# Kernel optimization log

Measured on AMD Instinct MI355X. Metric: run time of the kernel, lower is better.

## Reference

```python
import jax, jax.numpy as jnp
import numpy as np

B, NKV, NQ, D, H = 4, 2048, 1024, 1024, 16
HD = D // H


def setup_inputs() -> dict:
    key = jax.random.key(0)
    ks = jax.random.split(key, 9)
    s = 0.02
    return {
        "x": jax.random.normal(ks[0], (B, NKV, D), jnp.float32),
        "y": jax.random.normal(ks[1], (B, NQ, D), jnp.float32),
        "mask": jax.random.randint(ks[2], (B, NQ, NKV), 0, 2, jnp.int32),
        "W_kv": jax.random.normal(ks[3], (D, 2 * D), jnp.float32) * s,
        "b_kv": jnp.zeros((2 * D,), jnp.float32),
        "W_q": jax.random.normal(ks[4], (D, D), jnp.float32) * s,
        "b_q": jnp.zeros((D,), jnp.float32),
        "W_o": jax.random.normal(ks[5], (D, D), jnp.float32) * s,
        "b_o": jnp.zeros((D,), jnp.float32),
    }


def reference(x, y, mask, W_kv, b_kv, W_q, b_q, W_o, b_o):
    b, nkv, _ = x.shape
    nq = y.shape[1]
    kv = x @ W_kv + b_kv                                  # [B, NKV, 2D]
    q = y @ W_q + b_q                                     # [B, NQ, D]
    kv = kv.reshape(b, nkv, H, 2 * HD).transpose(0, 2, 1, 3)  # [B,H,NKV,2HD]
    q = q.reshape(b, nq, H, HD).transpose(0, 2, 1, 3)         # [B,H,NQ,HD]
    k, v = kv[..., :HD], kv[..., HD:]
    scores = jnp.einsum('bhqd,bhkd->bhqk', q, k) / jnp.sqrt(jnp.float32(HD))
    scores = jnp.where(mask[:, None, :, :] == 0, jnp.float32(-1e20), scores)
    attn = jax.nn.softmax(scores, axis=-1)
    vals = jnp.einsum('bhqk,bhkd->bhqd', attn, v)          # [B,H,NQ,HD]
    vals = vals.transpose(0, 2, 1, 3).reshape(b, nq, D)
    return vals @ W_o + b_o
```

## Files before the change

kernel.cpp:

```cpp
#include <hip/hip_runtime.h>
#include <hip/hip_bf16.h>
#include <math.h>

#define B_   4
#define NKV_ 2048
#define NQ_  1024
#define D_   1024
#define H_   16
#define HD_  64

typedef __attribute__((ext_vector_type(8))) short bf16x8;
typedef __attribute__((ext_vector_type(4))) float f32x4;

#define MFMA16x32(a, b, c) __builtin_amdgcn_mfma_f32_16x16x32_bf16((a), (b), (c), 0, 0, 0)

#define SC_LOG2 0.1803368801111244f

__device__ __forceinline__ short f2bf(float f) {
    unsigned u = __builtin_bit_cast(unsigned, f);
    u = (u + 0x7fff + ((u >> 16) & 1)) >> 16;
    return (short)u;
}
__device__ __forceinline__ unsigned cvt_pk_bf16(float lo, float hi) {
    unsigned r;
    asm("v_cvt_pk_bf16_f32 %0, %1, %2" : "=v"(r) : "v"(lo), "v"(hi));
    return r;
}
__device__ __forceinline__ void gload_lds16(const void* g, void* l) {
    __builtin_amdgcn_global_load_lds(
        (const __attribute__((address_space(1))) void*)g,
        (__attribute__((address_space(3))) void*)l, 16, 0, 0);
}

__global__ __launch_bounds__(256)
void cvt_hi2(const float* __restrict__ a, short* __restrict__ ah, int n4a,
             const float* __restrict__ bsrc, short* __restrict__ bh2, int n4b)
{
    const int ntot = n4a + n4b;
    for (int i = blockIdx.x * 256 + threadIdx.x; i < ntot; i += gridDim.x * 256) {
        const float4 v = (i < n4a)
            ? reinterpret_cast<const float4*>(a)[i]
            : reinterpret_cast<const float4*>(bsrc)[i - n4a];
        short4 h;
        h.x = f2bf(v.x);
        h.y = f2bf(v.y);
        h.z = f2bf(v.z);
        h.w = f2bf(v.w);
        if (i < n4a) reinterpret_cast<short4*>(ah)[i] = h;
        else         reinterpret_cast<short4*>(bh2)[i - n4a] = h;
    }
}

__global__ __launch_bounds__(256)
void splitT3(const float* __restrict__ Wkv, short* __restrict__ Tkv,
             const float* __restrict__ Wq,  short* __restrict__ Tq,
             const float* __restrict__ Wo,  short* __restrict__ To)
{
    const int bid = (int)blockIdx.x;
    const float* W; short* T; int K, N, bx, by;
    if (bid < 2048)      { W = Wkv; T = Tkv; K = D_; N = 2 * D_; bx = bid & 63;           by = bid >> 6; }
    else if (bid < 3072) { W = Wq;  T = Tq;  K = D_; N = D_;     bx = (bid - 2048) & 31;  by = (bid - 2048) >> 5; }
    else                 { W = Wo;  T = To;  K = D_; N = D_;     bx = (bid - 3072) & 31;  by = (bid - 3072) >> 5; }

    __shared__ float tile[32][33];
    const int tx = threadIdx.x & 31, ty = threadIdx.x >> 5;
    const int n0 = bx * 32, k0 = by * 32;
#pragma unroll
    for (int i = 0; i < 4; ++i)
        tile[ty + 8 * i][tx] = W[(size_t)(k0 + ty + 8 * i) * N + n0 + tx];
    __syncthreads();
#pragma unroll
    for (int i = 0; i < 4; ++i) {
        const float v = tile[tx][ty + 8 * i];
        T[(size_t)(n0 + ty + 8 * i) * K + k0 + tx] = f2bf(v);
    }
}

__global__ __launch_bounds__(256)
void maskpack16(const int* __restrict__ mask, unsigned short* __restrict__ m16,
                int nw)
{
    const int w = blockIdx.x * 256 + threadIdx.x;
    if (w >= nw) return;
    const int4* p = reinterpret_cast<const int4*>(mask + (size_t)w * 64);
    unsigned wg0 = 0, wg1 = 0, wg2 = 0, wg3 = 0;
#pragma unroll
    for (int i = 0; i < 16; ++i) {
        const int4 v = p[i];
        const unsigned nib = (unsigned)(v.x != 0) | ((unsigned)(v.y != 0) << 1)
                           | ((unsigned)(v.z != 0) << 2) | ((unsigned)(v.w != 0) << 3);
        const unsigned sh = 4u * (unsigned)(i >> 2);
        if ((i & 3) == 0) wg0 |= nib << sh;
        else if ((i & 3) == 1) wg1 |= nib << sh;
        else if ((i & 3) == 2) wg2 |= nib << sh;
        else wg3 |= nib << sh;
    }
    ushort4 o;
    o.x = (unsigned short)wg0; o.y = (unsigned short)wg1;
    o.z = (unsigned short)wg2; o.w = (unsigned short)wg3;
    reinterpret_cast<ushort4*>(m16)[w] = o;
}

template<int MODE>
__global__ __launch_bounds__(256)
void gemm1(const short* __restrict__ Ahi, const short* __restrict__ Bhi,
           const float* __restrict__ bias, void* __restrict__ out0,
           void* __restrict__ out1, int M, int N, int K)
{
    __shared__ short At[2][4096];
    __shared__ short Bt[2][4096];

    const int t    = threadIdx.x;
    const int wave = t >> 6;
    const int lane = t & 63;
    const int fr   = lane & 15;
    const int kq   = lane >> 4;

    const int gx  = N >> 7;
    const int gy  = M >> 7;
    const int lgx = __builtin_ctz(gx);
    const int bid = (int)blockIdx.x;
    const int xcd = bid & 7;
    const int j   = bid >> 3;
    const int m0  = (xcd * (gy >> 3) + (j >> lgx)) * 128;
    const int n0  = (j & (gx - 1)) * 128;

    const int wm0  = (wave & 1) * 64;
    const int wn0  = (wave >> 1) * 64;

    const int NT = K >> 5;

    const int r1 = t >> 2,         g1 = (t & 3) ^ ((r1 >> 1) & 3);
    const int r2 = (t + 256) >> 2, g2 = (t & 3) ^ ((r2 >> 1) & 3);

    f32x4 acc[4][4];
#pragma unroll
    for (int i = 0; i < 4; ++i)
#pragma unroll
        for (int j2 = 0; j2 < 4; ++j2) acc[i][j2] = f32x4{0.f, 0.f, 0.f, 0.f};

    auto stage = [&](int nb, int it) {
        const int kk = it << 5;
        gload_lds16(Ahi + (size_t)(m0 + r1) * K + kk + 8 * g1, &At[nb][wave * 512]);
        gload_lds16(Ahi + (size_t)(m0 + r2) * K + kk + 8 * g2, &At[nb][2048 + wave * 512]);
        gload_lds16(Bhi + (size_t)(n0 + r1) * K + kk + 8 * g1, &Bt[nb][wave * 512]);
        gload_lds16(Bhi + (size_t)(n0 + r2) * K + kk + 8 * g2, &Bt[nb][2048 + wave * 512]);
    };

    stage(0, 0);
    asm volatile("s_waitcnt vmcnt(0)" ::: "memory");
    __syncthreads();

    const int gsw = ((kq ^ ((fr >> 1) & 3)) << 3);
    int cur = 0;
    for (int it = 0; it < NT; ++it) {
        if (it + 1 < NT) stage(cur ^ 1, it + 1);
        bf16x8 af[4], bf[4];
#pragma unroll
        for (int i = 0; i < 4; ++i) {
            af[i] = *reinterpret_cast<const bf16x8*>(&At[cur][(wm0 + i * 16 + fr) * 32 + gsw]);
            bf[i] = *reinterpret_cast<const bf16x8*>(&Bt[cur][(wn0 + i * 16 + fr) * 32 + gsw]);
        }
        __builtin_amdgcn_s_setprio(1);
#pragma unroll
        for (int i = 0; i < 4; ++i)
#pragma unroll
            for (int j2 = 0; j2 < 4; ++j2)
                acc[i][j2] = MFMA16x32(af[i], bf[j2], acc[i][j2]);
        __builtin_amdgcn_s_setprio(0);
        asm volatile("s_waitcnt vmcnt(0)" ::: "memory");
        __syncthreads();
        cur ^= 1;
    }

#pragma unroll
    for (int i = 0; i < 4; ++i) {
#pragma unroll
        for (int j2 = 0; j2 < 4; ++j2) {
#pragma unroll
            for (int r = 0; r < 4; ++r) {
                const int m = m0 + wm0 + i * 16 + (lane >> 4) * 4 + r;
                const int n = n0 + wn0 + j2 * 16 + fr;
                const float v = acc[i][j2][r] + bias[n];
                if (MODE == 0) {
                    short* K_ = (short*)out0;
                    short* Vt = (short*)out1;
                    const int b  = m >> 11;
                    const int nk = m & 2047;
                    const int h  = n >> 7;
                    const int c  = n & 127;
                    const int bh = b * H_ + h;
                    if (c < 64)
                        K_[(((size_t)bh * NKV_ + nk) << 6) + c] = f2bf(v);
                    else
                        Vt[((size_t)bh * 64 + (c - 64)) * NKV_ + nk] = f2bf(v);
                } else if (MODE == 1) {
                    short* Q_ = (short*)out0;
                    const int b = m >> 10;
                    const int q = m & 1023;
                    const int h = n >> 6;
                    const int d = n & 63;
                    Q_[(((size_t)(b * H_ + h) * NQ_ + q) << 6) + d] =
                        f2bf(v * SC_LOG2);
                } else {
                    ((float*)out0)[(size_t)m * N + n] = v;
                }
            }
        }
    }
}

__global__ __launch_bounds__(512)
void attn_mfma(const short* __restrict__ Q, const short* __restrict__ K,
               const short* __restrict__ Vt,
               const unsigned short* __restrict__ m16,
               short* __restrict__ valshi)
{
    __shared__ short KtL[2][4096];
    __shared__ short VtL[2][4096];
    __shared__ short PsL[8192];

    const int t    = threadIdx.x;
    const int wave = t >> 6;
    const int lane = t & 63;
    const int fr   = lane & 15;
    const int g    = lane >> 4;

    const int bid = (int)blockIdx.x;
    const int xcd = bid & 7;
    const int j   = bid >> 3;
    const int bh  = xcd * 8 + (j >> 3);
    const int b   = bh >> 4;
    const int h   = bh & 15;
    const int wq0 = (j & 7) * 128 + wave * 16;

    const short* Kg  = K  + (size_t)bh * NKV_ * 64;
    const short* Vtg = Vt + (size_t)bh * 64 * NKV_;

    bf16x8 qf0, qf1;
    {
        const short* Qg = Q + ((size_t)bh * NQ_ + wq0 + fr) * 64 + g * 8;
        qf0 = *reinterpret_cast<const bf16x8*>(Qg);
        qf1 = *reinterpret_cast<const bf16x8*>(Qg + 32);
    }

    bf16x8 ones;
#pragma unroll
    for (int i = 0; i < 8; ++i) ones[i] = (short)0x3F80;

    f32x4 acc_o[4];
#pragma unroll
    for (int n = 0; n < 4; ++n) acc_o[n] = f32x4{0.f, 0.f, 0.f, 0.f};
    f32x4 lacc = f32x4{0.f, 0.f, 0.f, 0.f};

    const unsigned short* mbp =
        m16 + ((size_t)b * NQ_ + wq0 + fr) * (NKV_ / 64) * 4 + g;

    const int r8   = lane >> 3;
    const int csw  = ((lane & 7) << 3) ^ (r8 << 3);
    const int swzf = (fr & 7) << 3;
    short* PsW = PsL + wave * (16 * 64);

    auto stage = [&](int nb, int kt0) {
        const short* sK = Kg + (size_t)(kt0 + wave * 8 + r8) * 64 + csw;
        gload_lds16(sK, &KtL[nb][(wave * 8) * 64]);
        const short* sV = Vtg + (size_t)(wave * 8 + r8) * NKV_ + kt0 + csw;
        gload_lds16(sV, &VtL[nb][(wave * 8) * 64]);
    };

    stage(0, 0);
    asm volatile("s_waitcnt vmcnt(0)" ::: "memory");
    __syncthreads();

    const int kcol0 = (8 * g) ^ swzf;
    const int kcol1 = (32 + 8 * g) ^ swzf;

    int cur = 0;
    for (int kt = 0; kt < NKV_ / 64; ++kt) {
        if (kt + 1 < NKV_ / 64) stage(cur ^ 1, (kt + 1) * 64);

        const unsigned mskv = mbp[(size_t)kt * 4];

        const short* KB = &KtL[cur][fr * 64];
        f32x4 s_acc[4];
        __builtin_amdgcn_s_setprio(1);
#pragma unroll
        for (int t4 = 0; t4 < 4; ++t4) {
            s_acc[t4] = f32x4{0.f, 0.f, 0.f, 0.f};
            const bf16x8 kf0 = *reinterpret_cast<const bf16x8*>(KB + t4 * 1024 + kcol0);
            const bf16x8 kf1 = *reinterpret_cast<const bf16x8*>(KB + t4 * 1024 + kcol1);
            s_acc[t4] = MFMA16x32(kf0, qf0, s_acc[t4]);
            s_acc[t4] = MFMA16x32(kf1, qf1, s_acc[t4]);
        }
        __builtin_amdgcn_s_setprio(0);

        float p[16];
#pragma unroll
        for (int t4 = 0; t4 < 4; ++t4)
#pragma unroll
            for (int r = 0; r < 4; ++r) {
                const int i = 4 * t4 + r;
                const float e = __builtin_amdgcn_exp2f(s_acc[t4][r]);
                p[i] = ((mskv >> i) & 1u) ? e : 0.f;
            }

#pragma unroll
        for (int t4 = 0; t4 < 4; ++t4) {
            uint2 w;
            w.x = cvt_pk_bf16(p[4 * t4 + 0], p[4 * t4 + 1]);
            w.y = cvt_pk_bf16(p[4 * t4 + 2], p[4 * t4 + 3]);
            *reinterpret_cast<uint2*>(&PsW[fr * 64 + ((16 * t4 + 4 * g) ^ swzf)]) = w;
        }

        {
            const bf16x8 pf0 = *reinterpret_cast<const bf16x8*>(&PsW[fr * 64 + kcol0]);
            const bf16x8 pf1 = *reinterpret_cast<const bf16x8*>(&PsW[fr * 64 + kcol1]);
            const short* VB = &VtL[cur][fr * 64];
            __builtin_amdgcn_s_setprio(1);
            lacc = MFMA16x32(ones, pf0, lacc);
            lacc = MFMA16x32(ones, pf1, lacc);
#pragma unroll
            for (int n = 0; n < 4; ++n) {
                const bf16x8 vf0 = *reinterpret_cast<const bf16x8*>(VB + n * 1024 + kcol0);
                const bf16x8 vf1 = *reinterpret_cast<const bf16x8*>(VB + n * 1024 + kcol1);
                acc_o[n] = MFMA16x32(vf0, pf0, acc_o[n]);
                acc_o[n] = MFMA16x32(vf1, pf1, acc_o[n]);
            }
            __builtin_amdgcn_s_setprio(0);
        }

        asm volatile("s_waitcnt vmcnt(0)" ::: "memory");
        __syncthreads();
        cur ^= 1;
    }

    const float inv = 1.f / lacc[0];
    const size_t obase = ((size_t)b * NQ_ + wq0 + fr) * D_ + h * 64;
#pragma unroll
    for (int n = 0; n < 4; ++n) {
        short4 hh;
        hh.x = f2bf(acc_o[n][0] * inv);
        hh.y = f2bf(acc_o[n][1] * inv);
        hh.z = f2bf(acc_o[n][2] * inv);
        hh.w = f2bf(acc_o[n][3] * inv);
        *reinterpret_cast<short4*>(&valshi[obase + 16 * n + 4 * g]) = hh;
    }
}

extern "C" void kernel_launch(void* const* d_in, const int* in_sizes, int n_in,
                              void* d_out, int out_size, void* d_ws, size_t ws_size,
                              hipStream_t stream)
{
    const float* x    = (const float*)d_in[0];
    const float* y    = (const float*)d_in[1];
    const int*   mask = (const int*)  d_in[2];
    const float* W_kv = (const float*)d_in[3];
    const float* b_kv = (const float*)d_in[4];
    const float* W_q  = (const float*)d_in[5];
    const float* b_q  = (const float*)d_in[6];
    const float* W_o  = (const float*)d_in[7];
    const float* b_o  = (const float*)d_in[8];
    float* out = (float*)d_out;

    char* p = (char*)d_ws;
    auto take = [&](size_t bytes) { char* r = p; p += bytes; return r; };
    short* xhi    = (short*)take((size_t)B_ * NKV_ * D_ * 2);
    short* yhi    = (short*)take((size_t)B_ * NQ_ * D_ * 2);
    short* Wkvthi = (short*)take((size_t)2 * D_ * D_ * 2);
    short* Wqthi  = (short*)take((size_t)D_ * D_ * 2);
    short* Wothi  = (short*)take((size_t)D_ * D_ * 2);
    short* Kbf    = (short*)take((size_t)B_ * H_ * NKV_ * HD_ * 2);
    short* Vtbf   = (short*)take((size_t)B_ * H_ * HD_ * NKV_ * 2);
    short* Qbf    = (short*)take((size_t)B_ * H_ * NQ_ * HD_ * 2);
    unsigned short* m16 =
        (unsigned short*)take((size_t)B_ * NQ_ * (NKV_ / 64) * 4 * 2);
    short* valshi = xhi;

    cvt_hi2<<<2048, 256, 0, stream>>>(x, xhi, B_ * NKV_ * D_ / 4,
                                      y, yhi, B_ * NQ_ * D_ / 4);
    splitT3<<<4096, 256, 0, stream>>>(W_kv, Wkvthi, W_q, Wqthi, W_o, Wothi);
    maskpack16<<<(B_ * NQ_ * (NKV_ / 64)) / 256, 256, 0, stream>>>(
        mask, m16, B_ * NQ_ * (NKV_ / 64));

    gemm1<0><<<(2 * D_ / 128) * (B_ * NKV_ / 128), 256, 0, stream>>>(
        xhi, Wkvthi, b_kv, Kbf, Vtbf, B_ * NKV_, 2 * D_, D_);
    gemm1<1><<<(D_ / 128) * (B_ * NQ_ / 128), 256, 0, stream>>>(
        yhi, Wqthi, b_q, Qbf, nullptr, B_ * NQ_, D_, D_);

    attn_mfma<<<(NQ_ / 128) * (B_ * H_), 512, 0, stream>>>(
        Qbf, Kbf, Vtbf, m16, valshi);

    gemm1<2><<<(D_ / 128) * (B_ * NQ_ / 128), 256, 0, stream>>>(
        valshi, Wothi, b_o, out, nullptr, B_ * NQ_, D_, D_);

    (void)in_sizes; (void)n_in; (void)out_size; (void)ws_size;
}
```

Before: 186.8 us.

## Split attention over KV halves, merge prep kernels and projection GEMMs

Merges the three preprocessing kernels into one launch and the K/V and Q projection GEMMs into one launch. It also splits the attention KV loop into two halves to double the grid from 512 to 1024 blocks, so the GPU is better filled. A new combine kernel sums the unnormalized partial outputs and denominators, then writes the bf16 values. This adds fp32 partial-buffer traffic (two B×NQ×D arrays) and an extra launch. The split does no max rescaling, which the existing scaling scheme appears to allow.

```diff
diff --git a/kernel.cpp b/kernel.cpp
--- a/kernel.cpp
+++ b/kernel.cpp
@@ -33,79 +33,67 @@
 }
 
 __global__ __launch_bounds__(256)
-void cvt_hi2(const float* __restrict__ a, short* __restrict__ ah, int n4a,
-             const float* __restrict__ bsrc, short* __restrict__ bh2, int n4b)
-{
-    const int ntot = n4a + n4b;
-    for (int i = blockIdx.x * 256 + threadIdx.x; i < ntot; i += gridDim.x * 256) {
-        const float4 v = (i < n4a)
-            ? reinterpret_cast<const float4*>(a)[i]
-            : reinterpret_cast<const float4*>(bsrc)[i - n4a];
-        short4 h;
-        h.x = f2bf(v.x);
-        h.y = f2bf(v.y);
-        h.z = f2bf(v.z);
-        h.w = f2bf(v.w);
-        if (i < n4a) reinterpret_cast<short4*>(ah)[i] = h;
-        else         reinterpret_cast<short4*>(bh2)[i - n4a] = h;
-    }
-}
-
-__global__ __launch_bounds__(256)
-void splitT3(const float* __restrict__ Wkv, short* __restrict__ Tkv,
-             const float* __restrict__ Wq,  short* __restrict__ Tq,
-             const float* __restrict__ Wo,  short* __restrict__ To)
+void prep(const float* __restrict__ Wkv, short* __restrict__ Tkv,
+          const float* __restrict__ Wq,  short* __restrict__ Tq,
+          const float* __restrict__ Wo,  short* __restrict__ To,
+          const int* __restrict__ mask,  unsigned short* __restrict__ m16,
+          const float* __restrict__ x,   short* __restrict__ xh, int n4x,
+          const float* __restrict__ y,   short* __restrict__ yh, int n4y)
 {
     const int bid = (int)blockIdx.x;
-    const float* W; short* T; int K, N, bx, by;
-    if (bid < 2048)      { W = Wkv; T = Tkv; K = D_; N = 2 * D_; bx = bid & 63;           by = bid >> 6; }
-    else if (bid < 3072) { W = Wq;  T = Tq;  K = D_; N = D_;     bx = (bid - 2048) & 31;  by = (bid - 2048) >> 5; }
-    else                 { W = Wo;  T = To;  K = D_; N = D_;     bx = (bid - 3072) & 31;  by = (bid - 3072) >> 5; }
-
-    __shared__ float tile[32][33];
-    const int tx = threadIdx.x & 31, ty = threadIdx.x >> 5;
-    const int n0 = bx * 32, k0 = by * 32;
-#pragma unroll
-    for (int i = 0; i < 4; ++i)
-        tile[ty + 8 * i][tx] = W[(size_t)(k0 + ty + 8 * i) * N + n0 + tx];
-    __syncthreads();
-#pragma unroll
-    for (int i = 0; i < 4; ++i) {
-        const float v = tile[tx][ty + 8 * i];
-        T[(size_t)(n0 + ty + 8 * i) * K + k0 + tx] = f2bf(v);
-    }
-}
-
-__global__ __launch_bounds__(256)
-void maskpack16(const int* __restrict__ mask, unsigned short* __restrict__ m16,
-                int nw)
-{
-    const int w = blockIdx.x * 256 + threadIdx.x;
-    if (w >= nw) return;
-    const int4* p = reinterpret_cast<const int4*>(mask + (size_t)w * 64);
-    unsigned wg0 = 0, wg1 = 0, wg2 = 0, wg3 = 0;
-#pragma unroll
-    for (int i = 0; i < 16; ++i) {
-        const int4 v = p[i];
-        const unsigned nib = (unsigned)(v.x != 0) | ((unsigned)(v.y != 0) << 1)
-                           | ((unsigned)(v.z != 0) << 2) | ((unsigned)(v.w != 0) << 3);
-        const unsigned sh = 4u * (unsigned)(i >> 2);
-        if ((i & 3) == 0) wg0 |= nib << sh;
-        else if ((i & 3) == 1) wg1 |= nib << sh;
-        else if ((i & 3) == 2) wg2 |= nib << sh;
-        else wg3 |= nib << sh;
-    }
-    ushort4 o;
-    o.x = (unsigned short)wg0; o.y = (unsigned short)wg1;
-    o.z = (unsigned short)wg2; o.w = (unsigned short)wg3;
-    reinterpret_cast<ushort4*>(m16)[w] = o;
-}
-
-template<int MODE>
-__global__ __launch_bounds__(256)
-void gemm1(const short* __restrict__ Ahi, const short* __restrict__ Bhi,
-           const float* __restrict__ bias, void* __restrict__ out0,
-           void* __restrict__ out1, int M, int N, int K)
+    if (bid < 4096) {
+        const float* W; short* T; int K, N, bx, by;
+        if (bid < 2048)      { W = Wkv; T = Tkv; K = D_; N = 2 * D_; bx = bid & 63;          by = bid >> 6; }
+        else if (bid < 3072) { W = Wq;  T = Tq;  K = D_; N = D_;     bx = (bid - 2048) & 31; by = (bid - 2048) >> 5; }
+        else                 { W = Wo;  T = To;  K = D_; N = D_;     bx = (bid - 3072) & 31; by = (bid - 3072) >> 5; }
+        __shared__ float tile[32][33];
+        const int tx = threadIdx.x & 31, ty = threadIdx.x >> 5;
+        const int n0 = bx * 32, k0 = by * 32;
+#pragma unroll
+        for (int i = 0; i < 4; ++i)
+            tile[ty + 8 * i][tx] = W[(size_t)(k0 + ty + 8 * i) * N + n0 + tx];
+        __syncthreads();
+#pragma unroll
+        for (int i = 0; i < 4; ++i)
+            T[(size_t)(n0 + ty + 8 * i) * K + k0 + tx] = f2bf(tile[tx][ty + 8 * i]);
+    } else if (bid < 4608) {
+        const int w = (bid - 4096) * 256 + threadIdx.x;
+        const int4* pp = reinterpret_cast<const int4*>(mask + (size_t)w * 64);
+        unsigned wg0 = 0, wg1 = 0, wg2 = 0, wg3 = 0;
+#pragma unroll
+        for (int i = 0; i < 16; ++i) {
+            const int4 v = pp[i];
+            const unsigned nib = (unsigned)(v.x != 0) | ((unsigned)(v.y != 0) << 1)
+                               | ((unsigned)(v.z != 0) << 2) | ((unsigned)(v.w != 0) << 3);
+            const unsigned sh = 4u * (unsigned)(i >> 2);
+            if ((i & 3) == 0) wg0 |= nib << sh;
+            else if ((i & 3) == 1) wg1 |= nib << sh;
+            else if ((i & 3) == 2) wg2 |= nib << sh;
+            else wg3 |= nib << sh;
+        }
+        ushort4 o;
+        o.x = (unsigned short)wg0; o.y = (unsigned short)wg1;
+        o.z = (unsigned short)wg2; o.w = (unsigned short)wg3;
+        reinterpret_cast<ushort4*>(m16)[w] = o;
+    } else {
+        const int ntot = n4x + n4y;
+        for (int i = (bid - 4608) * 256 + threadIdx.x; i < ntot; i += 2048 * 256) {
+            const float4 v = (i < n4x)
+                ? reinterpret_cast<const float4*>(x)[i]
+                : reinterpret_cast<const float4*>(y)[i - n4x];
+            short4 h;
+            h.x = f2bf(v.x); h.y = f2bf(v.y); h.z = f2bf(v.z); h.w = f2bf(v.w);
+            if (i < n4x) reinterpret_cast<short4*>(xh)[i] = h;
+            else         reinterpret_cast<short4*>(yh)[i - n4x] = h;
+        }
+    }
+}
+
+__device__ __forceinline__
+void gemm_body(int mode, int bidl,
+               const short* __restrict__ Ahi, const short* __restrict__ Bhi,
+               const float* __restrict__ bias, void* __restrict__ out0,
+               void* __restrict__ out1, int M, int N, int K)
 {
     __shared__ short At[2][4096];
     __shared__ short Bt[2][4096];
@@ -119,16 +107,14 @@
     const int gx  = N >> 7;
     const int gy  = M >> 7;
     const int lgx = __builtin_ctz(gx);
-    const int bid = (int)blockIdx.x;
-    const int xcd = bid & 7;
-    const int j   = bid >> 3;
+    const int xcd = bidl & 7;
+    const int j   = bidl >> 3;
     const int m0  = (xcd * (gy >> 3) + (j >> lgx)) * 128;
     const int n0  = (j & (gx - 1)) * 128;
 
-    const int wm0  = (wave & 1) * 64;
-    const int wn0  = (wave >> 1) * 64;
-
-    const int NT = K >> 5;
+    const int wm0 = (wave & 1) * 64;
+    const int wn0 = (wave >> 1) * 64;
+    const int NT  = K >> 5;
 
     const int r1 = t >> 2,         g1 = (t & 3) ^ ((r1 >> 1) & 3);
     const int r2 = (t + 256) >> 2, g2 = (t & 3) ^ ((r2 >> 1) & 3);
@@ -182,7 +168,7 @@
                 const int m = m0 + wm0 + i * 16 + (lane >> 4) * 4 + r;
                 const int n = n0 + wn0 + j2 * 16 + fr;
                 const float v = acc[i][j2][r] + bias[n];
-                if (MODE == 0) {
+                if (mode == 0) {
                     short* K_ = (short*)out0;
                     short* Vt = (short*)out1;
                     const int b  = m >> 11;
@@ -194,7 +180,7 @@
                         K_[(((size_t)bh * NKV_ + nk) << 6) + c] = f2bf(v);
                     else
                         Vt[((size_t)bh * 64 + (c - 64)) * NKV_ + nk] = f2bf(v);
-                } else if (MODE == 1) {
+                } else if (mode == 1) {
                     short* Q_ = (short*)out0;
                     const int b = m >> 10;
                     const int q = m & 1023;
@@ -210,11 +196,32 @@
     }
 }
 
+__global__ __launch_bounds__(256)
+void proj(const short* __restrict__ xhi, const short* __restrict__ Wkvt,
+          const float* __restrict__ b_kv, short* __restrict__ Kbf,
+          short* __restrict__ Vtbf,
+          const short* __restrict__ yhi, const short* __restrict__ Wqt,
+          const float* __restrict__ b_q, short* __restrict__ Qbf)
+{
+    const int bid = (int)blockIdx.x;
+    if (bid < 1024)
+        gemm_body(0, bid, xhi, Wkvt, b_kv, Kbf, Vtbf, B_ * NKV_, 2 * D_, D_);
+    else
+        gemm_body(1, bid - 1024, yhi, Wqt, b_q, Qbf, nullptr, B_ * NQ_, D_, D_);
+}
+
+__global__ __launch_bounds__(256)
+void ogemm(const short* __restrict__ vals, const short* __restrict__ Wot,
+           const float* __restrict__ b_o, float* __restrict__ out)
+{
+    gemm_body(2, (int)blockIdx.x, vals, Wot, b_o, out, nullptr, B_ * NQ_, D_, D_);
+}
+
 __global__ __launch_bounds__(512)
 void attn_mfma(const short* __restrict__ Q, const short* __restrict__ K,
                const short* __restrict__ Vt,
                const unsigned short* __restrict__ m16,
-               short* __restrict__ valshi)
+               float* __restrict__ Opart, float* __restrict__ Lpart)
 {
     __shared__ short KtL[2][4096];
     __shared__ short VtL[2][4096];
@@ -226,13 +233,18 @@
     const int fr   = lane & 15;
     const int g    = lane >> 4;
 
-    const int bid = (int)blockIdx.x;
-    const int xcd = bid & 7;
-    const int j   = bid >> 3;
-    const int bh  = xcd * 8 + (j >> 3);
-    const int b   = bh >> 4;
-    const int h   = bh & 15;
-    const int wq0 = (j & 7) * 128 + wave * 16;
+    const int bid  = (int)blockIdx.x;
+    const int xcd  = bid & 7;
+    const int j    = bid >> 3;
+    const int bh   = xcd * 8 + (j >> 4);
+    const int rest = j & 15;
+    const int half = rest & 1;
+    const int b    = bh >> 4;
+    const int h    = bh & 15;
+    const int wq0  = (rest >> 1) * 128 + wave * 16;
+
+    const int kts = half * 16;
+    const int kte = kts + 16;
 
     const short* Kg  = K  + (size_t)bh * NKV_ * 64;
     const short* Vtg = Vt + (size_t)bh * 64 * NKV_;
@@ -268,7 +280,7 @@
         gload_lds16(sV, &VtL[nb][(wave * 8) * 64]);
     };
 
-    stage(0, 0);
+    stage(0, kts * 64);
     asm volatile("s_waitcnt vmcnt(0)" ::: "memory");
     __syncthreads();
 
@@ -276,8 +288,8 @@
     const int kcol1 = (32 + 8 * g) ^ swzf;
 
     int cur = 0;
-    for (int kt = 0; kt < NKV_ / 64; ++kt) {
-        if (kt + 1 < NKV_ / 64) stage(cur ^ 1, (kt + 1) * 64);
+    for (int kt = kts; kt < kte; ++kt) {
+        if (kt + 1 < kte) stage(cur ^ 1, (kt + 1) * 64);
 
         const unsigned mskv = mbp[(size_t)kt * 4];
 
@@ -334,16 +346,40 @@
         cur ^= 1;
     }
 
-    const float inv = 1.f / lacc[0];
+    float* Op = Opart + (size_t)half * (B_ * NQ_ * D_);
     const size_t obase = ((size_t)b * NQ_ + wq0 + fr) * D_ + h * 64;
 #pragma unroll
     for (int n = 0; n < 4; ++n) {
+        float4 v;
+        v.x = acc_o[n][0]; v.y = acc_o[n][1];
+        v.z = acc_o[n][2]; v.w = acc_o[n][3];
+        *reinterpret_cast<float4*>(&Op[obase + 16 * n + 4 * g]) = v;
+    }
+    if (g == 0)
+        Lpart[(size_t)half * (B_ * H_ * NQ_) + (size_t)bh * NQ_ + wq0 + fr] = lacc[0];
+}
+
+__global__ __launch_bounds__(256)
+void combine(const float* __restrict__ Opart, const float* __restrict__ Lpart,
+             short* __restrict__ valshi)
+{
+    const size_t npart = (size_t)B_ * NQ_ * D_;
+    const int n4 = (int)(npart / 4);
+    for (int i = blockIdx.x * 256 + threadIdx.x; i < n4; i += 2048 * 256) {
+        const int row  = i >> 8;
+        const int h    = (i & 255) >> 4;
+        const int b    = row >> 10;
+        const int q    = row & 1023;
+        const float4 o0 = reinterpret_cast<const float4*>(Opart)[i];
+        const float4 o1 = reinterpret_cast<const float4*>(Opart + npart)[i];
+        const size_t li = (size_t)(b * H_ + h) * NQ_ + q;
+        const float inv = 1.f / (Lpart[li] + Lpart[(size_t)B_ * H_ * NQ_ + li]);
         short4 hh;
-        hh.x = f2bf(acc_o[n][0] * inv);
-        hh.y = f2bf(acc_o[n][1] * inv);
-        hh.z = f2bf(acc_o[n][2] * inv);
-        hh.w = f2bf(acc_o[n][3] * inv);
-        *reinterpret_cast<short4*>(&valshi[obase + 16 * n + 4 * g]) = hh;
+        hh.x = f2bf((o0.x + o1.x) * inv);
+        hh.y = f2bf((o0.y + o1.y) * inv);
+        hh.z = f2bf((o0.z + o1.z) * inv);
+        hh.w = f2bf((o0.w + o1.w) * inv);
+        reinterpret_cast<short4*>(valshi)[i] = hh;
     }
 }
 
@@ -374,24 +410,23 @@
     short* Qbf    = (short*)take((size_t)B_ * H_ * NQ_ * HD_ * 2);
     unsigned short* m16 =
         (unsigned short*)take((size_t)B_ * NQ_ * (NKV_ / 64) * 4 * 2);
+    float* Opart  = (float*)take((size_t)2 * B_ * NQ_ * D_ * 4);
+    float* Lpart  = (float*)take((size_t)2 * B_ * H_ * NQ_ * 4);
     short* valshi = xhi;
 
-    cvt_hi2<<<2048, 256, 0, stream>>>(x, xhi, B_ * NKV_ * D_ / 4,
-                                      y, yhi, B_ * NQ_ * D_ / 4);
-    splitT3<<<4096, 256, 0, stream>>>(W_kv, Wkvthi, W_q, Wqthi, W_o, Wothi);
-    maskpack16<<<(B_ * NQ_ * (NKV_ / 64)) / 256, 256, 0, stream>>>(
-        mask, m16, B_ * NQ_ * (NKV_ / 64));
-
-    gemm1<0><<<(2 * D_ / 128) * (B_ * NKV_ / 128), 256, 0, stream>>>(
-        xhi, Wkvthi, b_kv, Kbf, Vtbf, B_ * NKV_, 2 * D_, D_);
-    gemm1<1><<<(D_ / 128) * (B_ * NQ_ / 128), 256, 0, stream>>>(
-        yhi, Wqthi, b_q, Qbf, nullptr, B_ * NQ_, D_, D_);
-
-    attn_mfma<<<(NQ_ / 128) * (B_ * H_), 512, 0, stream>>>(
-        Qbf, Kbf, Vtbf, m16, valshi);
-
-    gemm1<2><<<(D_ / 128) * (B_ * NQ_ / 128), 256, 0, stream>>>(
-        valshi, Wothi, b_o, out, nullptr, B_ * NQ_, D_, D_);
+    prep<<<6656, 256, 0, stream>>>(W_kv, Wkvthi, W_q, Wqthi, W_o, Wothi,
+                                   mask, m16,
+                                   x, xhi, B_ * NKV_ * D_ / 4,
+                                   y, yhi, B_ * NQ_ * D_ / 4);
+
+    proj<<<1280, 256, 0, stream>>>(xhi, Wkvthi, b_kv, Kbf, Vtbf,
+                                   yhi, Wqthi, b_q, Qbf);
+
+    attn_mfma<<<1024, 512, 0, stream>>>(Qbf, Kbf, Vtbf, m16, Opart, Lpart);
+
+    combine<<<2048, 256, 0, stream>>>(Opart, Lpart, valshi);
+
+    ogemm<<<256, 256, 0, stream>>>(valshi, Wothi, b_o, out);
 
     (void)in_sizes; (void)n_in; (void)out_size; (void)ws_size;
 }
```

Result: no change. 189.0 us (+1.2%).
